# Performance work log

Measured on AMD Instinct MI355X. Metric: run time of the kernel, lower is better.

## Reference

```python
import jax, jax.numpy as jnp
import numpy as np

N_HEAD = 8
N_EMBD = 512
HEAD_DIM = N_EMBD // N_HEAD


def setup_inputs() -> dict:
    key = jax.random.key(0)
    ks = jax.random.split(key, 9)
    B, S, D = 2, 4096, N_EMBD
    scale = 1.0 / np.sqrt(D)
    x = jax.random.normal(ks[0], (B, S, D), dtype=jnp.float32)
    Wq = jax.random.normal(ks[1], (D, D), dtype=jnp.float32) * scale
    bq = jax.random.normal(ks[2], (D,), dtype=jnp.float32) * 0.01
    Wk = jax.random.normal(ks[3], (D, D), dtype=jnp.float32) * scale
    bk = jax.random.normal(ks[4], (D,), dtype=jnp.float32) * 0.01
    Wv = jax.random.normal(ks[5], (D, D), dtype=jnp.float32) * scale
    bv = jax.random.normal(ks[6], (D,), dtype=jnp.float32) * 0.01
    Wo = jax.random.normal(ks[7], (D, D), dtype=jnp.float32) * scale
    bo = jax.random.normal(ks[8], (D,), dtype=jnp.float32) * 0.01
    return {"x": x, "Wq": Wq, "bq": bq, "Wk": Wk, "bk": bk,
            "Wv": Wv, "bv": bv, "Wo": Wo, "bo": bo}


def reference(x, Wq, bq, Wk, bk, Wv, bv, Wo, bo):
    B, S, D = x.shape
    H, Hd = N_HEAD, HEAD_DIM
    q = (x @ Wq + bq).reshape(B, S, H, Hd)
    k = (x @ Wk + bk).reshape(B, S, H, Hd)
    v = (x @ Wv + bv).reshape(B, S, H, Hd)
    # scores: [B, H, S, S]
    scores = jnp.einsum('bqhd,bkhd->bhqk', q, k) / jnp.sqrt(jnp.asarray(Hd, x.dtype))
    attn = jax.nn.softmax(scores, axis=-1)
    out = jnp.einsum('bhqk,bkhd->bqhd', attn, v).reshape(B, S, D)
    return out @ Wo + bo
```

## Files before the change

### kernel.cpp

```cpp
#include <hip/hip_runtime.h>

#define DEV static __device__ __forceinline__

using f32x4 = __attribute__((ext_vector_type(4))) float;
using s16x8 = __attribute__((ext_vector_type(8))) short;

DEV unsigned short f2bf(float x) {
    unsigned int u = __float_as_uint(x);
    unsigned int r = (u + 0x7FFFu + ((u >> 16) & 1u)) >> 16;
    return (unsigned short)r;
}
DEV float bf2f(unsigned short u) {
    return __uint_as_float(((unsigned int)u) << 16);
}

DEV f32x4 mfma16(s16x8 a, s16x8 b, f32x4 c) {
    return __builtin_amdgcn_mfma_f32_16x16x32_bf16(a, b, c, 0, 0, 0);
}

DEV unsigned cvtpk_bf16(float a, float b) {
    unsigned r;
    asm volatile("v_cvt_pk_bf16_f32 %0, %1, %2" : "=v"(r) : "v"(a), "v"(b));
    return r;
}

DEV void gload16(const unsigned short* g, short* l) {
    __builtin_amdgcn_global_load_lds(
        (const __attribute__((address_space(1))) unsigned int*)g,
        (__attribute__((address_space(3))) unsigned int*)l, 16, 0, 0);
}

#define LOG2E 1.4426950408889634f

__global__ void k_split(const float* __restrict__ in, unsigned short* __restrict__ hi,
                        unsigned short* __restrict__ lo, int n4) {
    for (int i = blockIdx.x * blockDim.x + threadIdx.x; i < n4; i += gridDim.x * blockDim.x) {
        float4 v = ((const float4*)in)[i];
        ushort4 h, l;
        h.x = f2bf(v.x); l.x = f2bf(v.x - bf2f(h.x));
        h.y = f2bf(v.y); l.y = f2bf(v.y - bf2f(h.y));
        h.z = f2bf(v.z); l.z = f2bf(v.z - bf2f(h.z));
        h.w = f2bf(v.w); l.w = f2bf(v.w - bf2f(h.w));
        ((ushort4*)hi)[i] = h;
        ((ushort4*)lo)[i] = l;
    }
}

__global__ void k_wfuse(const float* __restrict__ Wq, const float* __restrict__ Wk,
                        const float* __restrict__ Wv, const float* __restrict__ Wo,
                        const float* __restrict__ bq, const float* __restrict__ bk,
                        const float* __restrict__ bv,
                        unsigned short* __restrict__ WBhi, unsigned short* __restrict__ WBlo,
                        unsigned short* __restrict__ Wothi, unsigned short* __restrict__ Wotlo,
                        float* __restrict__ bcat, float qs) {
    __shared__ float tile[64][65];
    int blk = blockIdx.x;
    if (blk >= 256) {
        int i = (blk - 256) * 256 + threadIdx.x;
        bcat[i] = (i < 512) ? bq[i] * qs : (i < 1024) ? bk[i - 512] : bv[i - 1024];
        return;
    }
    int wi = blk >> 6, sub = blk & 63;
    const float* W = (wi == 0) ? Wq : (wi == 1) ? Wk : (wi == 2) ? Wv : Wo;
    float scale = (wi == 0) ? qs : 1.0f;
    unsigned short* Thi = (wi < 3) ? WBhi + (size_t)wi * 512 * 512 : Wothi;
    unsigned short* Tlo = (wi < 3) ? WBlo + (size_t)wi * 512 * 512 : Wotlo;
    int bk0 = (sub >> 3) * 64, bn = (sub & 7) * 64;
    int t = threadIdx.x;
    int r = t >> 2, c4 = (t & 3) * 16;
#pragma unroll
    for (int j = 0; j < 16; j += 4) {
        float4 v = *(const float4*)&W[(size_t)(bk0 + r) * 512 + bn + c4 + j];
        tile[r][c4 + j + 0] = v.x; tile[r][c4 + j + 1] = v.y;
        tile[r][c4 + j + 2] = v.z; tile[r][c4 + j + 3] = v.w;
    }
    __syncthreads();
    int n = t >> 2, k4 = (t & 3) * 16;
#pragma unroll
    for (int j = 0; j < 16; ++j) {
        float x = tile[k4 + j][n] * scale;
        unsigned short h = f2bf(x);
        Thi[(size_t)(bn + n) * 512 + bk0 + k4 + j] = h;
        Tlo[(size_t)(bn + n) * 512 + bk0 + k4 + j] = f2bf(x - bf2f(h));
    }
}

template <int MODE>
__global__ __launch_bounds__(256, 3) void k_gemm2(
    const unsigned short* __restrict__ Ahi, const unsigned short* __restrict__ Alo,
    const unsigned short* __restrict__ Bhi, const unsigned short* __restrict__ Blo,
    const float* __restrict__ bias,
    unsigned short* __restrict__ Qh,
    unsigned short* __restrict__ Kh,
    unsigned short* __restrict__ Vt,
    float* __restrict__ Cf) {
    __shared__ short As[128 * 64];
    __shared__ short Bs[128 * 64];
    int t = threadIdx.x, lane = t & 63, w = t >> 6;
    int wr = w >> 1, wc = w & 1, lr = lane & 15, lg = lane >> 4;
    int bm = blockIdx.y * 128, bn = blockIdx.x * 128;
    f32x4 acc[4][4] = {};
    int srow = t >> 3;
    int sc = t & 7;
    int gcol = (sc ^ (srow & 7)) * 8;
    int axr = (lr & 7) * 8;
    const int NC = (MODE == 0) ? 24 : 16;
    for (int c = 0; c < NC; ++c) {
        int seg = c >> 3, kb = (c & 7) * 64;
        const unsigned short* Ap, * Bp;
        if (MODE == 0) {
            Ap = (seg < 2) ? Ahi : Alo;
            Bp = (seg == 1) ? Blo : Bhi;
        } else {
            Ap = Ahi;
            Bp = seg ? Blo : Bhi;
        }
        const unsigned short* ag = Ap + (size_t)(bm + srow) * 512 + kb + gcol;
        const unsigned short* bg = Bp + (size_t)(bn + srow) * 512 + kb + gcol;
#pragma unroll
        for (int ps = 0; ps < 4; ++ps) {
            gload16(ag + (size_t)ps * 32 * 512, &As[(srow + ps * 32) * 64 + sc * 8]);
            gload16(bg + (size_t)ps * 32 * 512, &Bs[(srow + ps * 32) * 64 + sc * 8]);
        }
        __syncthreads();
#pragma unroll
        for (int kk = 0; kk < 2; ++kk) {
            s16x8 af[4], bf[4];
#pragma unroll
            for (int i = 0; i < 4; ++i)
                af[i] = *(const s16x8*)&As[(wr * 64 + i * 16 + lr) * 64 + ((kk * 32 + lg * 8) ^ axr)];
#pragma unroll
            for (int i = 0; i < 4; ++i)
                bf[i] = *(const s16x8*)&Bs[(wc * 64 + i * 16 + lr) * 64 + ((kk * 32 + lg * 8) ^ axr)];
#pragma unroll
            for (int i = 0; i < 4; ++i)
#pragma unroll
                for (int j = 0; j < 4; ++j) acc[i][j] = mfma16(af[i], bf[j], acc[i][j]);
        }
        __syncthreads();
    }
    int sel = bn >> 9;
#pragma unroll
    for (int i = 0; i < 4; ++i)
#pragma unroll
        for (int j = 0; j < 4; ++j) {
            int m = bm + wr * 64 + i * 16 + lg * 4;
            int n0 = bn + wc * 64 + j * 16;
            float bv = bias[n0 + lr];
            if (MODE == 1) {
#pragma unroll
                for (int r = 0; r < 4; ++r)
                    Cf[(size_t)(m + r) * 512 + n0 + lr] = acc[i][j][r] + bv;
            } else if (sel < 2) {
                int col = (n0 & 511) + lr;
                unsigned short* Ph = sel ? Kh : Qh;
#pragma unroll
                for (int r = 0; r < 4; ++r)
                    Ph[(size_t)(m + r) * 512 + col] = f2bf(acc[i][j][r] + bv);
            } else {
                int nc = (n0 & 511) + lr;
                int bidx = m >> 12, s = m & 4095;
                size_t row = ((size_t)bidx * 8 + (nc >> 6)) * 64 + (nc & 63);
                uint2 pv;
                pv.x = cvtpk_bf16(acc[i][j][0] + bv, acc[i][j][1] + bv);
                pv.y = cvtpk_bf16(acc[i][j][2] + bv, acc[i][j][3] + bv);
                *(uint2*)&Vt[row * 4096 + s] = pv;
            }
        }
}

__global__ __launch_bounds__(512, 2) void k_attn(
    const unsigned short* __restrict__ Qhi,
    const unsigned short* __restrict__ Khi,
    const unsigned short* __restrict__ Vthi,
    unsigned short* __restrict__ Ohi) {
    __shared__ short L[27648];
    short* Kls = &L[0];
    short* Vls = &L[4608];
    int t = threadIdx.x, lane = t & 63, w = t >> 6;
    int lr = lane & 15, lg = lane >> 4;
    int bid = blockIdx.x;
    int swz = (bid & 7) * 32 + (bid >> 3);
    int bh = swz >> 4, qt = swz & 15;
    int b = bh >> 3, h = bh & 7;
    int qbase = qt * 256 + w * 32;
    short* pw = &L[9216 + w * 2304];

    s16x8 qr[2][2];
#pragma unroll
    for (int qf = 0; qf < 2; ++qf) {
        size_t mrow = (size_t)(b * 4096 + qbase + qf * 16 + lr) * 512 + h * 64;
        qr[qf][0] = *(const s16x8*)&Qhi[mrow + lg * 8];
        qr[qf][1] = *(const s16x8*)&Qhi[mrow + 32 + lg * 8];
    }

    f32x4 oacc[4][2] = {};
    float mrun[2] = {-1e30f, -1e30f}, lrun[2] = {0.f, 0.f};

    int krow = t >> 3, kc = (t & 7) * 8;
    const unsigned short* Kb = Khi + (size_t)(b * 4096 + krow) * 512 + h * 64 + kc;
    const unsigned short* Vb = Vthi + (size_t)(bh * 64 + krow) * 4096 + kc;
    s16x8 k0 = *(const s16x8*)Kb;
    s16x8 v0 = *(const s16x8*)Vb;

    for (int kt = 0; kt < 64; ++kt) {
        *(s16x8*)&Kls[krow * 72 + kc] = k0;
        *(s16x8*)&Vls[krow * 72 + kc] = v0;
        {
            int ktn = (kt < 63) ? kt + 1 : 63;
            k0 = *(const s16x8*)(Kb + (size_t)ktn * 64 * 512);
            v0 = *(const s16x8*)(Vb + ktn * 64);
        }
        __syncthreads();

        f32x4 sacc[4][2] = {};
        __builtin_amdgcn_s_setprio(1);
#pragma unroll
        for (int kk = 0; kk < 2; ++kk)
#pragma unroll
            for (int kf = 0; kf < 4; ++kf) {
                s16x8 af = *(const s16x8*)&Kls[(kf * 16 + lr) * 72 + kk * 32 + lg * 8];
                sacc[kf][0] = mfma16(af, qr[0][kk], sacc[kf][0]);
                sacc[kf][1] = mfma16(af, qr[1][kk], sacc[kf][1]);
            }
        __builtin_amdgcn_s_setprio(0);

#pragma unroll
        for (int qf = 0; qf < 2; ++qf) {
            float tmax = -1e30f;
#pragma unroll
            for (int kf = 0; kf < 4; ++kf)
#pragma unroll
                for (int r = 0; r < 4; ++r) tmax = fmaxf(tmax, sacc[kf][qf][r]);
            tmax = fmaxf(tmax, __shfl_xor(tmax, 16));
            tmax = fmaxf(tmax, __shfl_xor(tmax, 32));
            if (!__all(tmax <= mrun[qf] + 4.0f)) {
                float mnew = fmaxf(mrun[qf], tmax);
                float alpha = exp2f(mrun[qf] - mnew);
                mrun[qf] = mnew;
                lrun[qf] *= alpha;
#pragma unroll
                for (int df = 0; df < 4; ++df) oacc[df][qf] *= alpha;
            }
            float m = mrun[qf];
            float tsum = 0.f;
#pragma unroll
            for (int kf = 0; kf < 4; ++kf)
#pragma unroll
                for (int r = 0; r < 4; ++r) {
                    float pv = exp2f(sacc[kf][qf][r] - m);
                    sacc[kf][qf][r] = pv;
                    tsum += pv;
                }
            tsum += __shfl_xor(tsum, 16);
            tsum += __shfl_xor(tsum, 32);
            lrun[qf] += tsum;

            int q = qf * 16 + lr;
#pragma unroll
            for (int kf = 0; kf < 4; ++kf) {
                uint2 hv;
                hv.x = cvtpk_bf16(sacc[kf][qf][0], sacc[kf][qf][1]);
                hv.y = cvtpk_bf16(sacc[kf][qf][2], sacc[kf][qf][3]);
                *(uint2*)&pw[q * 72 + kf * 16 + lg * 4] = hv;
            }
        }

        s16x8 pfr[2][2];
#pragma unroll
        for (int qf = 0; qf < 2; ++qf)
#pragma unroll
            for (int vv = 0; vv < 2; ++vv)
                pfr[qf][vv] = *(const s16x8*)&pw[(qf * 16 + lr) * 72 + vv * 32 + lg * 8];
        __builtin_amdgcn_s_setprio(1);
#pragma unroll
        for (int vv = 0; vv < 2; ++vv)
#pragma unroll
            for (int df = 0; df < 4; ++df) {
                s16x8 vf = *(const s16x8*)&Vls[(df * 16 + lr) * 72 + vv * 32 + lg * 8];
                oacc[df][0] = mfma16(vf, pfr[0][vv], oacc[df][0]);
                oacc[df][1] = mfma16(vf, pfr[1][vv], oacc[df][1]);
            }
        __builtin_amdgcn_s_setprio(0);
        __syncthreads();
    }

    float inv[2] = {1.f / lrun[0], 1.f / lrun[1]};
    float* ow = (float*)&L[0] + w * 1088;
#pragma unroll
    for (int pp = 0; pp < 2; ++pp) {
        if (pp) __syncthreads();
#pragma unroll
        for (int df = 0; df < 4; ++df) {
            f32x4 v = oacc[df][pp] * inv[pp];
            *(f32x4*)&ow[lr * 68 + df * 16 + lg * 4] = v;
        }
        int q = lane >> 2, dc = (lane & 3) * 16;
        f32x4 x0 = *(f32x4*)&ow[q * 68 + dc];
        f32x4 x1 = *(f32x4*)&ow[q * 68 + dc + 4];
        f32x4 x2 = *(f32x4*)&ow[q * 68 + dc + 8];
        f32x4 x3 = *(f32x4*)&ow[q * 68 + dc + 12];
        uint4 h0, h1;
        h0.x = cvtpk_bf16(x0[0], x0[1]); h0.y = cvtpk_bf16(x0[2], x0[3]);
        h0.z = cvtpk_bf16(x1[0], x1[1]); h0.w = cvtpk_bf16(x1[2], x1[3]);
        h1.x = cvtpk_bf16(x2[0], x2[1]); h1.y = cvtpk_bf16(x2[2], x2[3]);
        h1.z = cvtpk_bf16(x3[0], x3[1]); h1.w = cvtpk_bf16(x3[2], x3[3]);
        size_t gbase = (size_t)(b * 4096 + qbase + pp * 16 + q) * 512 + h * 64 + dc;
        *(uint4*)&Ohi[gbase] = h0;
        *(uint4*)&Ohi[gbase + 8] = h1;
    }
}

extern "C" void kernel_launch(void* const* d_in, const int* in_sizes, int n_in,
                              void* d_out, int out_size, void* d_ws, size_t ws_size,
                              hipStream_t stream) {
    const float* x  = (const float*)d_in[0];
    const float* Wq = (const float*)d_in[1];
    const float* bq = (const float*)d_in[2];
    const float* Wk = (const float*)d_in[3];
    const float* bk = (const float*)d_in[4];
    const float* Wv = (const float*)d_in[5];
    const float* bv = (const float*)d_in[6];
    const float* Wo = (const float*)d_in[7];
    const float* bo = (const float*)d_in[8];
    float* out = (float*)d_out;

    char* ws = (char*)d_ws;
    const size_t PLANE = (size_t)8192 * 512 * 2;
    const size_t WBPL  = (size_t)1536 * 512 * 2;
    const size_t WPL   = (size_t)512 * 512 * 2;
    size_t off = 0;
    unsigned short* Xhi   = (unsigned short*)(ws + off); off += PLANE;
    unsigned short* Xlo   = (unsigned short*)(ws + off); off += PLANE;
    unsigned short* WBhi  = (unsigned short*)(ws + off); off += WBPL;
    unsigned short* WBlo  = (unsigned short*)(ws + off); off += WBPL;
    unsigned short* Wothi = (unsigned short*)(ws + off); off += WPL;
    unsigned short* Wotlo = (unsigned short*)(ws + off); off += WPL;
    float*          bcat  = (float*)(ws + off);          off += 1536 * 4;
    unsigned short* Qhi   = (unsigned short*)(ws + off); off += PLANE;
    unsigned short* Khi   = (unsigned short*)(ws + off); off += PLANE;
    unsigned short* Vthi  = (unsigned short*)(ws + off); off += PLANE;
    unsigned short* Ohi = Xhi;

    const float QS = 0.125f * LOG2E;

    k_split<<<1024, 256, 0, stream>>>(x, Xhi, Xlo, 8192 * 512 / 4);
    k_wfuse<<<262, 256, 0, stream>>>(Wq, Wk, Wv, Wo, bq, bk, bv,
                                     WBhi, WBlo, Wothi, Wotlo, bcat, QS);
    k_gemm2<0><<<dim3(12, 64), 256, 0, stream>>>(Xhi, Xlo, WBhi, WBlo, bcat,
                                                 Qhi, Khi, Vthi, nullptr);
    k_attn<<<256, 512, 0, stream>>>(Qhi, Khi, Vthi, Ohi);
    k_gemm2<1><<<dim3(4, 64), 256, 0, stream>>>(Ohi, nullptr, Wothi, Wotlo, bo,
                                                nullptr, nullptr, nullptr, out);
}
```

Measured before the change: 312.3 us.

## Split attention KV range across two blocks with merge kernel; narrower out-proj tiles

The attention kernel now splits each query tile's key range into two halves handled by separate blocks (512 blocks instead of 256). Each block writes fp32 partial outputs plus running max and sum, and a new merge kernel combines them into the bf16 attention output. The row-sum is now accumulated with an MFMA against a ones vector instead of shuffles. The output projection GEMM is templated on N-tile width and launched with 64-wide tiles to get more blocks. The aim is better CU occupancy on a grid that previously filled only 256 blocks, at the cost of extra partial-result memory traffic and one more kernel launch.

```diff
diff --git a/kernel.cpp b/kernel.cpp
--- a/kernel.cpp
+++ b/kernel.cpp
@@ -85,7 +85,7 @@
     }
 }
 
-template <int MODE>
+template <int MODE, int BNT>
 __global__ __launch_bounds__(256, 3) void k_gemm2(
     const unsigned short* __restrict__ Ahi, const unsigned short* __restrict__ Alo,
     const unsigned short* __restrict__ Bhi, const unsigned short* __restrict__ Blo,
@@ -94,12 +94,13 @@
     unsigned short* __restrict__ Kh,
     unsigned short* __restrict__ Vt,
     float* __restrict__ Cf) {
+    constexpr int NJ = BNT / 32;
     __shared__ short As[128 * 64];
-    __shared__ short Bs[128 * 64];
+    __shared__ short Bs[BNT * 64];
     int t = threadIdx.x, lane = t & 63, w = t >> 6;
     int wr = w >> 1, wc = w & 1, lr = lane & 15, lg = lane >> 4;
-    int bm = blockIdx.y * 128, bn = blockIdx.x * 128;
-    f32x4 acc[4][4] = {};
+    int bm = blockIdx.y * 128, bn = blockIdx.x * BNT;
+    f32x4 acc[4][NJ] = {};
     int srow = t >> 3;
     int sc = t & 7;
     int gcol = (sc ^ (srow & 7)) * 8;
@@ -118,24 +119,25 @@
         const unsigned short* ag = Ap + (size_t)(bm + srow) * 512 + kb + gcol;
         const unsigned short* bg = Bp + (size_t)(bn + srow) * 512 + kb + gcol;
 #pragma unroll
-        for (int ps = 0; ps < 4; ++ps) {
+        for (int ps = 0; ps < 4; ++ps)
             gload16(ag + (size_t)ps * 32 * 512, &As[(srow + ps * 32) * 64 + sc * 8]);
+#pragma unroll
+        for (int ps = 0; ps < BNT / 32; ++ps)
             gload16(bg + (size_t)ps * 32 * 512, &Bs[(srow + ps * 32) * 64 + sc * 8]);
-        }
         __syncthreads();
 #pragma unroll
         for (int kk = 0; kk < 2; ++kk) {
-            s16x8 af[4], bf[4];
+            s16x8 af[4], bf[NJ];
 #pragma unroll
             for (int i = 0; i < 4; ++i)
                 af[i] = *(const s16x8*)&As[(wr * 64 + i * 16 + lr) * 64 + ((kk * 32 + lg * 8) ^ axr)];
 #pragma unroll
+            for (int j = 0; j < NJ; ++j)
+                bf[j] = *(const s16x8*)&Bs[(wc * (BNT / 2) + j * 16 + lr) * 64 + ((kk * 32 + lg * 8) ^ axr)];
+#pragma unroll
             for (int i = 0; i < 4; ++i)
-                bf[i] = *(const s16x8*)&Bs[(wc * 64 + i * 16 + lr) * 64 + ((kk * 32 + lg * 8) ^ axr)];
-#pragma unroll
-            for (int i = 0; i < 4; ++i)
-#pragma unroll
-                for (int j = 0; j < 4; ++j) acc[i][j] = mfma16(af[i], bf[j], acc[i][j]);
+#pragma unroll
+                for (int j = 0; j < NJ; ++j) acc[i][j] = mfma16(af[i], bf[j], acc[i][j]);
         }
         __syncthreads();
     }
@@ -143,9 +145,9 @@
 #pragma unroll
     for (int i = 0; i < 4; ++i)
 #pragma unroll
-        for (int j = 0; j < 4; ++j) {
+        for (int j = 0; j < NJ; ++j) {
             int m = bm + wr * 64 + i * 16 + lg * 4;
-            int n0 = bn + wc * 64 + j * 16;
+            int n0 = bn + wc * (BNT / 2) + j * 16;
             float bv = bias[n0 + lr];
             if (MODE == 1) {
 #pragma unroll
@@ -173,15 +175,17 @@
     const unsigned short* __restrict__ Qhi,
     const unsigned short* __restrict__ Khi,
     const unsigned short* __restrict__ Vthi,
-    unsigned short* __restrict__ Ohi) {
+    float* __restrict__ Op, float* __restrict__ Mp, float* __restrict__ Lp) {
     __shared__ short L[27648];
     short* Kls = &L[0];
     short* Vls = &L[4608];
     int t = threadIdx.x, lane = t & 63, w = t >> 6;
     int lr = lane & 15, lg = lane >> 4;
     int bid = blockIdx.x;
-    int swz = (bid & 7) * 32 + (bid >> 3);
-    int bh = swz >> 4, qt = swz & 15;
+    int swz = (bid & 7) * 64 + (bid >> 3);
+    int half = swz & 1;
+    int rest = swz >> 1;
+    int bh = rest >> 4, qt = rest & 15;
     int b = bh >> 3, h = bh & 7;
     int qbase = qt * 256 + w * 32;
     short* pw = &L[9216 + w * 2304];
@@ -193,21 +197,26 @@
         qr[qf][0] = *(const s16x8*)&Qhi[mrow + lg * 8];
         qr[qf][1] = *(const s16x8*)&Qhi[mrow + 32 + lg * 8];
     }
+    s16x8 ones;
+#pragma unroll
+    for (int j = 0; j < 8; ++j) ones[j] = (short)0x3F80;
 
     f32x4 oacc[4][2] = {};
-    float mrun[2] = {-1e30f, -1e30f}, lrun[2] = {0.f, 0.f};
+    f32x4 lacc[2] = {};
+    float mrun[2] = {-1e30f, -1e30f};
 
     int krow = t >> 3, kc = (t & 7) * 8;
     const unsigned short* Kb = Khi + (size_t)(b * 4096 + krow) * 512 + h * 64 + kc;
     const unsigned short* Vb = Vthi + (size_t)(bh * 64 + krow) * 4096 + kc;
-    s16x8 k0 = *(const s16x8*)Kb;
-    s16x8 v0 = *(const s16x8*)Vb;
-
-    for (int kt = 0; kt < 64; ++kt) {
+    int kt0 = half * 32, ktend = kt0 + 32;
+    s16x8 k0 = *(const s16x8*)(Kb + (size_t)kt0 * 64 * 512);
+    s16x8 v0 = *(const s16x8*)(Vb + kt0 * 64);
+
+    for (int kt = kt0; kt < ktend; ++kt) {
         *(s16x8*)&Kls[krow * 72 + kc] = k0;
         *(s16x8*)&Vls[krow * 72 + kc] = v0;
         {
-            int ktn = (kt < 63) ? kt + 1 : 63;
+            int ktn = (kt < ktend - 1) ? kt + 1 : ktend - 1;
             k0 = *(const s16x8*)(Kb + (size_t)ktn * 64 * 512);
             v0 = *(const s16x8*)(Vb + ktn * 64);
         }
@@ -238,23 +247,16 @@
                 float mnew = fmaxf(mrun[qf], tmax);
                 float alpha = exp2f(mrun[qf] - mnew);
                 mrun[qf] = mnew;
-                lrun[qf] *= alpha;
+                lacc[qf] *= alpha;
 #pragma unroll
                 for (int df = 0; df < 4; ++df) oacc[df][qf] *= alpha;
             }
             float m = mrun[qf];
-            float tsum = 0.f;
 #pragma unroll
             for (int kf = 0; kf < 4; ++kf)
 #pragma unroll
-                for (int r = 0; r < 4; ++r) {
-                    float pv = exp2f(sacc[kf][qf][r] - m);
-                    sacc[kf][qf][r] = pv;
-                    tsum += pv;
-                }
-            tsum += __shfl_xor(tsum, 16);
-            tsum += __shfl_xor(tsum, 32);
-            lrun[qf] += tsum;
+                for (int r = 0; r < 4; ++r)
+                    sacc[kf][qf][r] = exp2f(sacc[kf][qf][r] - m);
 
             int q = qf * 16 + lr;
 #pragma unroll
@@ -274,41 +276,68 @@
                 pfr[qf][vv] = *(const s16x8*)&pw[(qf * 16 + lr) * 72 + vv * 32 + lg * 8];
         __builtin_amdgcn_s_setprio(1);
 #pragma unroll
-        for (int vv = 0; vv < 2; ++vv)
+        for (int vv = 0; vv < 2; ++vv) {
 #pragma unroll
             for (int df = 0; df < 4; ++df) {
                 s16x8 vf = *(const s16x8*)&Vls[(df * 16 + lr) * 72 + vv * 32 + lg * 8];
                 oacc[df][0] = mfma16(vf, pfr[0][vv], oacc[df][0]);
                 oacc[df][1] = mfma16(vf, pfr[1][vv], oacc[df][1]);
             }
+            lacc[0] = mfma16(ones, pfr[0][vv], lacc[0]);
+            lacc[1] = mfma16(ones, pfr[1][vv], lacc[1]);
+        }
         __builtin_amdgcn_s_setprio(0);
         __syncthreads();
     }
 
-    float inv[2] = {1.f / lrun[0], 1.f / lrun[1]};
     float* ow = (float*)&L[0] + w * 1088;
 #pragma unroll
     for (int pp = 0; pp < 2; ++pp) {
         if (pp) __syncthreads();
 #pragma unroll
-        for (int df = 0; df < 4; ++df) {
-            f32x4 v = oacc[df][pp] * inv[pp];
-            *(f32x4*)&ow[lr * 68 + df * 16 + lg * 4] = v;
-        }
+        for (int df = 0; df < 4; ++df)
+            *(f32x4*)&ow[lr * 68 + df * 16 + lg * 4] = oacc[df][pp];
         int q = lane >> 2, dc = (lane & 3) * 16;
-        f32x4 x0 = *(f32x4*)&ow[q * 68 + dc];
-        f32x4 x1 = *(f32x4*)&ow[q * 68 + dc + 4];
-        f32x4 x2 = *(f32x4*)&ow[q * 68 + dc + 8];
-        f32x4 x3 = *(f32x4*)&ow[q * 68 + dc + 12];
-        uint4 h0, h1;
-        h0.x = cvtpk_bf16(x0[0], x0[1]); h0.y = cvtpk_bf16(x0[2], x0[3]);
-        h0.z = cvtpk_bf16(x1[0], x1[1]); h0.w = cvtpk_bf16(x1[2], x1[3]);
-        h1.x = cvtpk_bf16(x2[0], x2[1]); h1.y = cvtpk_bf16(x2[2], x2[3]);
-        h1.z = cvtpk_bf16(x3[0], x3[1]); h1.w = cvtpk_bf16(x3[2], x3[3]);
-        size_t gbase = (size_t)(b * 4096 + qbase + pp * 16 + q) * 512 + h * 64 + dc;
-        *(uint4*)&Ohi[gbase] = h0;
-        *(uint4*)&Ohi[gbase + 8] = h1;
-    }
+        size_t qglob = (size_t)bh * 4096 + qbase + pp * 16 + q;
+        float* dst = Op + ((size_t)half * 65536 + qglob) * 64 + dc;
+        *(f32x4*)(dst + 0)  = *(f32x4*)&ow[q * 68 + dc + 0];
+        *(f32x4*)(dst + 4)  = *(f32x4*)&ow[q * 68 + dc + 4];
+        *(f32x4*)(dst + 8)  = *(f32x4*)&ow[q * 68 + dc + 8];
+        *(f32x4*)(dst + 12) = *(f32x4*)&ow[q * 68 + dc + 12];
+        if (lane < 16) {
+            size_t qg = (size_t)half * 65536 + (size_t)bh * 4096 + qbase + pp * 16 + lane;
+            Mp[qg] = mrun[pp];
+            Lp[qg] = lacc[pp][0];
+        }
+    }
+}
+
+__global__ void k_merge(const float* __restrict__ Op, const float* __restrict__ Mp,
+                        const float* __restrict__ Lp, unsigned short* __restrict__ Ohi) {
+    int t = blockIdx.x * 256 + threadIdx.x;
+    int q = t >> 2, dc = (t & 3) * 16;
+    float m0 = Mp[q], m1 = Mp[65536 + q];
+    float l0 = Lp[q], l1 = Lp[65536 + q];
+    float M = fmaxf(m0, m1);
+    float w0 = exp2f(m0 - M), w1 = exp2f(m1 - M);
+    float inv = 1.0f / (w0 * l0 + w1 * l1);
+    w0 *= inv; w1 *= inv;
+    const float* p0 = Op + (size_t)q * 64 + dc;
+    const float* p1 = p0 + (size_t)65536 * 64;
+    int bh = q >> 12, s = q & 4095;
+    size_t gbase = ((size_t)((bh >> 3) * 4096 + s)) * 512 + (bh & 7) * 64 + dc;
+    uint4 o0, o1;
+    f32x4 a, b, r;
+    a = *(const f32x4*)(p0 + 0);  b = *(const f32x4*)(p1 + 0);  r = a * w0 + b * w1;
+    o0.x = cvtpk_bf16(r[0], r[1]); o0.y = cvtpk_bf16(r[2], r[3]);
+    a = *(const f32x4*)(p0 + 4);  b = *(const f32x4*)(p1 + 4);  r = a * w0 + b * w1;
+    o0.z = cvtpk_bf16(r[0], r[1]); o0.w = cvtpk_bf16(r[2], r[3]);
+    a = *(const f32x4*)(p0 + 8);  b = *(const f32x4*)(p1 + 8);  r = a * w0 + b * w1;
+    o1.x = cvtpk_bf16(r[0], r[1]); o1.y = cvtpk_bf16(r[2], r[3]);
+    a = *(const f32x4*)(p0 + 12); b = *(const f32x4*)(p1 + 12); r = a * w0 + b * w1;
+    o1.z = cvtpk_bf16(r[0], r[1]); o1.w = cvtpk_bf16(r[2], r[3]);
+    *(uint4*)&Ohi[gbase] = o0;
+    *(uint4*)&Ohi[gbase + 8] = o1;
 }
 
 extern "C" void kernel_launch(void* const* d_in, const int* in_sizes, int n_in,
@@ -340,6 +369,9 @@
     unsigned short* Qhi   = (unsigned short*)(ws + off); off += PLANE;
     unsigned short* Khi   = (unsigned short*)(ws + off); off += PLANE;
     unsigned short* Vthi  = (unsigned short*)(ws + off); off += PLANE;
+    float*          Opart = (float*)(ws + off);          off += (size_t)2 * 65536 * 64 * 4;
+    float*          Mpart = (float*)(ws + off);          off += (size_t)2 * 65536 * 4;
+    float*          Lpart = (float*)(ws + off);          off += (size_t)2 * 65536 * 4;
     unsigned short* Ohi = Xhi;
 
     const float QS = 0.125f * LOG2E;
@@ -347,9 +379,10 @@
     k_split<<<1024, 256, 0, stream>>>(x, Xhi, Xlo, 8192 * 512 / 4);
     k_wfuse<<<262, 256, 0, stream>>>(Wq, Wk, Wv, Wo, bq, bk, bv,
                                      WBhi, WBlo, Wothi, Wotlo, bcat, QS);
-    k_gemm2<0><<<dim3(12, 64), 256, 0, stream>>>(Xhi, Xlo, WBhi, WBlo, bcat,
-                                                 Qhi, Khi, Vthi, nullptr);
-    k_attn<<<256, 512, 0, stream>>>(Qhi, Khi, Vthi, Ohi);
-    k_gemm2<1><<<dim3(4, 64), 256, 0, stream>>>(Ohi, nullptr, Wothi, Wotlo, bo,
-                                                nullptr, nullptr, nullptr, out);
-}
+    k_gemm2<0, 128><<<dim3(12, 64), 256, 0, stream>>>(Xhi, Xlo, WBhi, WBlo, bcat,
+                                                      Qhi, Khi, Vthi, nullptr);
+    k_attn<<<512, 512, 0, stream>>>(Qhi, Khi, Vthi, Opart, Mpart, Lpart);
+    k_merge<<<1024, 256, 0, stream>>>(Opart, Mpart, Lpart, Ohi);
+    k_gemm2<1, 64><<<dim3(8, 64), 256, 0, stream>>>(Ohi, nullptr, Wothi, Wotlo, bo,
+                                                    nullptr, nullptr, nullptr, out);
+}
```

New measurement: 328.9 us. +5.3%, slower.
